# Performance work log

Hardware: AMD Instinct MI355X
Metric: run time of the kernel (lower is better)

## Reference

```python
import jax, jax.numpy as jnp
import numpy as np

B, N, E = 64, 256, 8192


def setup_inputs() -> dict:
    key = jax.random.key(0)
    k1, k2, k3, k4, k5 = jax.random.split(key, 5)
    P = jax.random.uniform(k1, (B, N, N), dtype=jnp.float32)
    d_error = jax.random.uniform(k2, (N, N), dtype=jnp.float32)
    edge_i = jax.random.randint(k3, (B, E), 0, N, dtype=jnp.int32)
    edge_j = jax.random.randint(k4, (B, E), 0, N, dtype=jnp.int32)
    edge_w = jax.random.uniform(k5, (B, E), dtype=jnp.float32)
    return {"P": P, "d_error": d_error, "edge_i": edge_i,
            "edge_j": edge_j, "edge_w": edge_w}


def reference(P, d_error, edge_i, edge_j, edge_w):
    # cost_e = P[b, i_e, :] @ d_error @ P[b, j_e, :]
    # Precompute Q = P @ d_error once, then gather per edge (memory-bound).
    Q = jnp.einsum('bin,nm->bim', P, d_error)            # [B, N, N]
    Qi = jnp.take_along_axis(Q, edge_i[:, :, None], axis=1)   # [B, E, N]
    Pj = jnp.take_along_axis(P, edge_j[:, :, None], axis=1)   # [B, E, N]
    cost = jnp.sum(Qi * Pj, axis=-1)                      # [B, E]
    sample_loss = jnp.sum(edge_w * cost, axis=-1)         # [B]
    sample_weight = jnp.maximum(jnp.sum(edge_w, axis=-1), 1e-8)
    # every sample has edges -> valid_samples == B, i.e. a mean over batch
    return jnp.mean(sample_loss / sample_weight)
```

## Files before the change

kernel.cpp:

```cpp
#include <hip/hip_runtime.h>

#define NN 256
#define BB 64
#define EE 8192

typedef __attribute__((ext_vector_type(8))) short bf16x8;
typedef __attribute__((ext_vector_type(8))) unsigned short u16x8;
typedef __attribute__((ext_vector_type(4))) float f32x4;

__device__ __forceinline__ unsigned short f2bf(float f) {
  union { float f; unsigned u; } x; x.f = f;
  unsigned r = x.u + 0x7FFFu + ((x.u >> 16) & 1u);
  return (unsigned short)(r >> 16);
}

__device__ __forceinline__ float bf2f(unsigned short h) {
  union { unsigned u; float f; } x; x.u = ((unsigned)h) << 16;
  return x.f;
}

__global__ __launch_bounds__(256) void transposeD(const float* __restrict__ D,
                                                  unsigned short* __restrict__ Dt) {
  __shared__ float t[32][33];
  int bx = blockIdx.x & 7;
  int by = blockIdx.x >> 3;
  int c = threadIdx.x & 31, r0 = threadIdx.x >> 5;
#pragma unroll
  for (int p = 0; p < 4; ++p) {
    int row = r0 + p * 8;
    t[row][c] = D[(bx * 32 + row) * NN + by * 32 + c];
  }
  __syncthreads();
#pragma unroll
  for (int p = 0; p < 4; ++p) {
    int row = r0 + p * 8;
    Dt[(by * 32 + row) * NN + bx * 32 + c] = f2bf(t[c][row]);
  }
}

__global__ __launch_bounds__(256) void gemm1(const float* __restrict__ P,
                                             const unsigned short* __restrict__ Dt,
                                             unsigned short* __restrict__ Qbf) {
  __shared__ __align__(16) unsigned short As[4096];
  __shared__ __align__(16) unsigned short Bs[4096];
  const int tid = threadIdx.x;
  const int b = blockIdx.x >> 2;
  const int tile = blockIdx.x & 3;
  const int ty = tile >> 1, tx = tile & 1;
  const int rowBase = ty * 128, colBase = tx * 128;

  const float4* Ag4 = (const float4*)(P + b * NN * NN);

  f32x4 acc[4][4];
#pragma unroll
  for (int i = 0; i < 4; ++i)
#pragma unroll
    for (int j = 0; j < 4; ++j) acc[i][j] = (f32x4){0.f, 0.f, 0.f, 0.f};

  const int lane = tid & 63;
  const int wave = tid >> 6;
  const int wr = (wave >> 1) * 64, wc = (wave & 1) * 64;
  const int frm = lane & 15;
  const int fq = (lane >> 4) * 8;

  const int arow0 = tid >> 3, af4 = tid & 7;
  const int brow0 = tid >> 2, bch = tid & 3;

  float4 ra[4];
  u16x8 rb[2];
#pragma unroll
  for (int i = 0; i < 4; ++i)
    ra[i] = Ag4[(rowBase + arow0 + i * 32) * 64 + 0 * 8 + af4];
#pragma unroll
  for (int i = 0; i < 2; ++i)
    rb[i] = *(const u16x8*)(Dt + (colBase + brow0 + i * 64) * NN + 0 * 32 + bch * 8);

  for (int ks = 0; ks < 8; ++ks) {
    __syncthreads();
#pragma unroll
    for (int i = 0; i < 4; ++i) {
      ushort4 o;
      o.x = f2bf(ra[i].x); o.y = f2bf(ra[i].y); o.z = f2bf(ra[i].z); o.w = f2bf(ra[i].w);
      *(ushort4*)(As + (arow0 + i * 32) * 32 + af4 * 4) = o;
    }
#pragma unroll
    for (int i = 0; i < 2; ++i)
      *(u16x8*)(Bs + (brow0 + i * 64) * 32 + bch * 8) = rb[i];
    __syncthreads();
    if (ks < 7) {
      const int k0 = (ks + 1) * 32;
#pragma unroll
      for (int i = 0; i < 4; ++i)
        ra[i] = Ag4[(rowBase + arow0 + i * 32) * 64 + (k0 >> 2) + af4];
#pragma unroll
      for (int i = 0; i < 2; ++i)
        rb[i] = *(const u16x8*)(Dt + (colBase + brow0 + i * 64) * NN + k0 + bch * 8);
    }
    bf16x8 af[4], bfr[4];
#pragma unroll
    for (int t = 0; t < 4; ++t) {
      af[t]  = *(const bf16x8*)(As + (wr + t * 16 + frm) * 32 + fq);
      bfr[t] = *(const bf16x8*)(Bs + (wc + t * 16 + frm) * 32 + fq);
    }
#pragma unroll
    for (int tr = 0; tr < 4; ++tr)
#pragma unroll
      for (int tc = 0; tc < 4; ++tc)
        acc[tr][tc] = __builtin_amdgcn_mfma_f32_16x16x32_bf16(af[tr], bfr[tc],
                                                              acc[tr][tc], 0, 0, 0);
  }

  unsigned short* outB = Qbf + b * NN * NN;
#pragma unroll
  for (int tr = 0; tr < 4; ++tr)
#pragma unroll
    for (int tc = 0; tc < 4; ++tc)
#pragma unroll
      for (int r = 0; r < 4; ++r) {
        int rg = rowBase + wr + tr * 16 + (lane >> 4) * 4 + r;
        int cg = colBase + wc + tc * 16 + (lane & 15);
        outB[rg * NN + cg] = f2bf(acc[tr][tc][r]);
      }
}

__global__ __launch_bounds__(256) void gemm2_fused(const unsigned short* __restrict__ Qbf,
                                                   const float* __restrict__ P,
                                                   const int* __restrict__ ei,
                                                   const int* __restrict__ ej,
                                                   const float* __restrict__ ew,
                                                   float* __restrict__ out) {
  __shared__ __align__(16) unsigned short As[4096];
  __shared__ __align__(16) unsigned short Bs[4096];
  __shared__ __align__(16) unsigned short Mt[128 * 130];
  __shared__ float red[8];
  const int tid = threadIdx.x;
  const int b = blockIdx.x >> 2;
  const int tile = blockIdx.x & 3;
  const int ty = tile >> 1, tx = tile & 1;
  const int rowBase = ty * 128, colBase = tx * 128;

  const unsigned short* Ag = Qbf + b * NN * NN;
  const float4* Bg4 = (const float4*)(P + b * NN * NN);

  f32x4 acc[4][4];
#pragma unroll
  for (int i = 0; i < 4; ++i)
#pragma unroll
    for (int j = 0; j < 4; ++j) acc[i][j] = (f32x4){0.f, 0.f, 0.f, 0.f};

  const int lane = tid & 63;
  const int wave = tid >> 6;
  const int wr = (wave >> 1) * 64, wc = (wave & 1) * 64;
  const int frm = lane & 15;
  const int fq = (lane >> 4) * 8;

  const int arow0 = tid >> 2, ach = tid & 3;
  const int brow0 = tid >> 3, bf4 = tid & 7;

  u16x8 ra[2];
  float4 rb[4];
#pragma unroll
  for (int i = 0; i < 2; ++i)
    ra[i] = *(const u16x8*)(Ag + (rowBase + arow0 + i * 64) * NN + ach * 8);
#pragma unroll
  for (int i = 0; i < 4; ++i)
    rb[i] = Bg4[(colBase + brow0 + i * 32) * 64 + bf4];

  for (int ks = 0; ks < 8; ++ks) {
    __syncthreads();
#pragma unroll
    for (int i = 0; i < 2; ++i)
      *(u16x8*)(As + (arow0 + i * 64) * 32 + ach * 8) = ra[i];
#pragma unroll
    for (int i = 0; i < 4; ++i) {
      ushort4 o;
      o.x = f2bf(rb[i].x); o.y = f2bf(rb[i].y); o.z = f2bf(rb[i].z); o.w = f2bf(rb[i].w);
      *(ushort4*)(Bs + (brow0 + i * 32) * 32 + bf4 * 4) = o;
    }
    __syncthreads();
    if (ks < 7) {
      const int k0 = (ks + 1) * 32;
#pragma unroll
      for (int i = 0; i < 2; ++i)
        ra[i] = *(const u16x8*)(Ag + (rowBase + arow0 + i * 64) * NN + k0 + ach * 8);
#pragma unroll
      for (int i = 0; i < 4; ++i)
        rb[i] = Bg4[(colBase + brow0 + i * 32) * 64 + (k0 >> 2) + bf4];
    }
    bf16x8 af[4], bfr[4];
#pragma unroll
    for (int t = 0; t < 4; ++t) {
      af[t]  = *(const bf16x8*)(As + (wr + t * 16 + frm) * 32 + fq);
      bfr[t] = *(const bf16x8*)(Bs + (wc + t * 16 + frm) * 32 + fq);
    }
#pragma unroll
    for (int tr = 0; tr < 4; ++tr)
#pragma unroll
      for (int tc = 0; tc < 4; ++tc)
        acc[tr][tc] = __builtin_amdgcn_mfma_f32_16x16x32_bf16(af[tr], bfr[tc],
                                                              acc[tr][tc], 0, 0, 0);
  }

#pragma unroll
  for (int tr = 0; tr < 4; ++tr)
#pragma unroll
    for (int tc = 0; tc < 4; ++tc)
#pragma unroll
      for (int r = 0; r < 4; ++r) {
        int rl = wr + tr * 16 + (lane >> 4) * 4 + r;
        int cl = wc + tc * 16 + (lane & 15);
        Mt[rl * 130 + cl] = f2bf(acc[tr][tc][r]);
      }
  __syncthreads();

  float lsum = 0.f, wsum = 0.f;
  const int2*   ei2 = (const int2*)(ei + b * EE);
  const int2*   ej2 = (const int2*)(ej + b * EE);
  const float2* ew2 = (const float2*)(ew + b * EE);
#pragma unroll 4
  for (int s = 0; s < 16; ++s) {
    int idx = s * 256 + tid;
    int2 ii = ei2[idx];
    int2 jj = ej2[idx];
    float2 ww = ew2[idx];
    wsum += ww.x + ww.y;
    int il = ii.x - rowBase, jl = jj.x - colBase;
    if (((unsigned)il < 128u) && ((unsigned)jl < 128u))
      lsum += ww.x * bf2f(Mt[il * 130 + jl]);
    il = ii.y - rowBase; jl = jj.y - colBase;
    if (((unsigned)il < 128u) && ((unsigned)jl < 128u))
      lsum += ww.y * bf2f(Mt[il * 130 + jl]);
  }
#pragma unroll
  for (int o = 32; o; o >>= 1) {
    lsum += __shfl_down(lsum, o);
    wsum += __shfl_down(wsum, o);
  }
  if (lane == 0) { red[wave] = lsum; red[4 + wave] = wsum; }
  __syncthreads();
  if (tid == 0) {
    float l = red[0] + red[1] + red[2] + red[3];
    float w = red[4] + red[5] + red[6] + red[7];
    atomicAdd(out, l / (64.0f * fmaxf(w, 1e-8f)));
  }
}

extern "C" void kernel_launch(void* const* d_in, const int* in_sizes, int n_in,
                              void* d_out, int out_size, void* d_ws, size_t ws_size,
                              hipStream_t stream) {
  const float* P  = (const float*)d_in[0];
  const float* D  = (const float*)d_in[1];
  const int*   ei = (const int*)d_in[2];
  const int*   ej = (const int*)d_in[3];
  const float* ew = (const float*)d_in[4];
  float* out = (float*)d_out;

  char* ws = (char*)d_ws;
  unsigned short* Qbf = (unsigned short*)ws;
  unsigned short* Dt  = (unsigned short*)(ws + 8388608);

  hipMemsetAsync(out, 0, out_size * sizeof(float), stream);
  transposeD<<<64, 256, 0, stream>>>(D, Dt);
  gemm1<<<256, 256, 0, stream>>>(P, Dt, Qbf);
  gemm2_fused<<<256, 256, 0, stream>>>(Qbf, P, ei, ej, ew, out);
}
```

Baseline: 102.5 us.

## Fuse both GEMMs into one kernel keeping Q tile in shared memory

Merges gemm1 and gemm2_fused into a single kernel. Each block computes its 128x256 strip of Q = P·D in registers and stores it as bf16 in LDS, then multiplies by the P^T tile and gathers edges from LDS. This removes the Q round-trip through global memory and one launch. The memset is folded into the transpose kernel, and edge loads are widened to int4. In exchange, each block recomputes the Q rows shared with its sibling tile, doubling the first GEMM's work. The larger LDS footprint and accumulator set limit occupancy to one block per CU.

New measurement: 97.21 us. -5.2%, faster.

```diff
diff --git a/kernel.cpp b/kernel.cpp
--- a/kernel.cpp
+++ b/kernel.cpp
@@ -3,6 +3,7 @@
 #define NN 256
 #define BB 64
 #define EE 8192
+#define TS_LD 264
 
 typedef __attribute__((ext_vector_type(8))) short bf16x8;
 typedef __attribute__((ext_vector_type(8))) unsigned short u16x8;
@@ -20,7 +21,9 @@
 }
 
 __global__ __launch_bounds__(256) void transposeD(const float* __restrict__ D,
-                                                  unsigned short* __restrict__ Dt) {
+                                                  unsigned short* __restrict__ Dt,
+                                                  float* __restrict__ out) {
+  if (blockIdx.x == 0 && threadIdx.x == 0) out[0] = 0.0f;
   __shared__ float t[32][33];
   int bx = blockIdx.x & 7;
   int by = blockIdx.x >> 3;
@@ -38,44 +41,54 @@
   }
 }
 
-__global__ __launch_bounds__(256) void gemm1(const float* __restrict__ P,
-                                             const unsigned short* __restrict__ Dt,
-                                             unsigned short* __restrict__ Qbf) {
-  __shared__ __align__(16) unsigned short As[4096];
-  __shared__ __align__(16) unsigned short Bs[4096];
+__global__ __launch_bounds__(256, 1) void fused(const float* __restrict__ P,
+                                                const unsigned short* __restrict__ Dt,
+                                                const int* __restrict__ ei,
+                                                const int* __restrict__ ej,
+                                                const float* __restrict__ ew,
+                                                float* __restrict__ out) {
+  __shared__ __align__(16) unsigned short As[128 * 32];
+  __shared__ __align__(16) unsigned short Bs[256 * 32];
+  __shared__ __align__(16) unsigned short Ts[128 * TS_LD];
+  __shared__ float red[8];
+
   const int tid = threadIdx.x;
   const int b = blockIdx.x >> 2;
   const int tile = blockIdx.x & 3;
   const int ty = tile >> 1, tx = tile & 1;
   const int rowBase = ty * 128, colBase = tx * 128;
 
-  const float4* Ag4 = (const float4*)(P + b * NN * NN);
-
-  f32x4 acc[4][4];
-#pragma unroll
-  for (int i = 0; i < 4; ++i)
-#pragma unroll
-    for (int j = 0; j < 4; ++j) acc[i][j] = (f32x4){0.f, 0.f, 0.f, 0.f};
-
   const int lane = tid & 63;
   const int wave = tid >> 6;
   const int wr = (wave >> 1) * 64, wc = (wave & 1) * 64;
   const int frm = lane & 15;
   const int fq = (lane >> 4) * 8;
+  const int crow = (lane >> 4) * 4;
+  const int ccol = lane & 15;
+
+  const float4* Pb4 = (const float4*)(P + b * NN * NN);
 
   const int arow0 = tid >> 3, af4 = tid & 7;
   const int brow0 = tid >> 2, bch = tid & 3;
 
+  f32x4 acc[4][8];
+#pragma unroll
+  for (int i = 0; i < 4; ++i)
+#pragma unroll
+    for (int j = 0; j < 8; ++j) acc[i][j] = (f32x4){0.f, 0.f, 0.f, 0.f};
+
   float4 ra[4];
-  u16x8 rb[2];
-#pragma unroll
-  for (int i = 0; i < 4; ++i)
-    ra[i] = Ag4[(rowBase + arow0 + i * 32) * 64 + 0 * 8 + af4];
-#pragma unroll
-  for (int i = 0; i < 2; ++i)
-    rb[i] = *(const u16x8*)(Dt + (colBase + brow0 + i * 64) * NN + 0 * 32 + bch * 8);
-
-  for (int ks = 0; ks < 8; ++ks) {
+  u16x8 rb[4];
+  float4 pb[4];
+#pragma unroll
+  for (int i = 0; i < 4; ++i)
+    ra[i] = Pb4[(rowBase + arow0 + i * 32) * 64 + af4];
+#pragma unroll
+  for (int i = 0; i < 4; ++i)
+    rb[i] = *(const u16x8*)(Dt + (brow0 + i * 64) * NN + bch * 8);
+
+  for (int s = 0; s < 8; ++s) {
+    const int k0 = s * 32;
     __syncthreads();
 #pragma unroll
     for (int i = 0; i < 4; ++i) {
@@ -84,22 +97,76 @@
       *(ushort4*)(As + (arow0 + i * 32) * 32 + af4 * 4) = o;
     }
 #pragma unroll
-    for (int i = 0; i < 2; ++i)
+    for (int i = 0; i < 4; ++i)
       *(u16x8*)(Bs + (brow0 + i * 64) * 32 + bch * 8) = rb[i];
     __syncthreads();
-    if (ks < 7) {
-      const int k0 = (ks + 1) * 32;
-#pragma unroll
-      for (int i = 0; i < 4; ++i)
-        ra[i] = Ag4[(rowBase + arow0 + i * 32) * 64 + (k0 >> 2) + af4];
-#pragma unroll
-      for (int i = 0; i < 2; ++i)
-        rb[i] = *(const u16x8*)(Dt + (colBase + brow0 + i * 64) * NN + k0 + bch * 8);
+    if (s < 7) {
+      const int k1 = k0 + 32;
+#pragma unroll
+      for (int i = 0; i < 4; ++i)
+        ra[i] = Pb4[(rowBase + arow0 + i * 32) * 64 + (k1 >> 2) + af4];
+#pragma unroll
+      for (int i = 0; i < 4; ++i)
+        rb[i] = *(const u16x8*)(Dt + (brow0 + i * 64) * NN + k1 + bch * 8);
+    } else {
+#pragma unroll
+      for (int i = 0; i < 4; ++i)
+        pb[i] = Pb4[(colBase + arow0 + i * 32) * 64 + af4];
+    }
+    bf16x8 af[4], bfr[8];
+#pragma unroll
+    for (int t = 0; t < 4; ++t)
+      af[t] = *(const bf16x8*)(As + (wr + t * 16 + frm) * 32 + fq);
+#pragma unroll
+    for (int h = 0; h < 2; ++h)
+#pragma unroll
+      for (int t = 0; t < 4; ++t)
+        bfr[h * 4 + t] = *(const bf16x8*)(Bs + (h * 128 + wc + t * 16 + frm) * 32 + fq);
+#pragma unroll
+    for (int tr = 0; tr < 4; ++tr)
+#pragma unroll
+      for (int j = 0; j < 8; ++j)
+        acc[tr][j] = __builtin_amdgcn_mfma_f32_16x16x32_bf16(af[tr], bfr[j],
+                                                             acc[tr][j], 0, 0, 0);
+  }
+
+#pragma unroll
+  for (int tr = 0; tr < 4; ++tr)
+#pragma unroll
+    for (int h = 0; h < 2; ++h)
+#pragma unroll
+      for (int tc = 0; tc < 4; ++tc)
+#pragma unroll
+        for (int r = 0; r < 4; ++r) {
+          int rl = wr + tr * 16 + crow + r;
+          int cl = h * 128 + wc + tc * 16 + ccol;
+          Ts[rl * TS_LD + cl] = f2bf(acc[tr][h * 4 + tc][r]);
+        }
+
+#pragma unroll
+  for (int i = 0; i < 4; ++i)
+#pragma unroll
+    for (int j = 0; j < 4; ++j) acc[i][j] = (f32x4){0.f, 0.f, 0.f, 0.f};
+
+  for (int s = 0; s < 8; ++s) {
+    const int k0 = s * 32;
+    __syncthreads();
+#pragma unroll
+    for (int i = 0; i < 4; ++i) {
+      ushort4 o;
+      o.x = f2bf(pb[i].x); o.y = f2bf(pb[i].y); o.z = f2bf(pb[i].z); o.w = f2bf(pb[i].w);
+      *(ushort4*)(Bs + (arow0 + i * 32) * 32 + af4 * 4) = o;
+    }
+    __syncthreads();
+    if (s < 7) {
+#pragma unroll
+      for (int i = 0; i < 4; ++i)
+        pb[i] = Pb4[(colBase + arow0 + i * 32) * 64 + ((k0 + 32) >> 2) + af4];
     }
     bf16x8 af[4], bfr[4];
 #pragma unroll
     for (int t = 0; t < 4; ++t) {
-      af[t]  = *(const bf16x8*)(As + (wr + t * 16 + frm) * 32 + fq);
+      af[t]  = *(const bf16x8*)(Ts + (wr + t * 16 + frm) * TS_LD + k0 + fq);
       bfr[t] = *(const bf16x8*)(Bs + (wc + t * 16 + frm) * 32 + fq);
     }
 #pragma unroll
@@ -110,126 +177,38 @@
                                                               acc[tr][tc], 0, 0, 0);
   }
 
-  unsigned short* outB = Qbf + b * NN * NN;
 #pragma unroll
   for (int tr = 0; tr < 4; ++tr)
 #pragma unroll
     for (int tc = 0; tc < 4; ++tc)
 #pragma unroll
       for (int r = 0; r < 4; ++r) {
-        int rg = rowBase + wr + tr * 16 + (lane >> 4) * 4 + r;
-        int cg = colBase + wc + tc * 16 + (lane & 15);
-        outB[rg * NN + cg] = f2bf(acc[tr][tc][r]);
-      }
-}
-
-__global__ __launch_bounds__(256) void gemm2_fused(const unsigned short* __restrict__ Qbf,
-                                                   const float* __restrict__ P,
-                                                   const int* __restrict__ ei,
-                                                   const int* __restrict__ ej,
-                                                   const float* __restrict__ ew,
-                                                   float* __restrict__ out) {
-  __shared__ __align__(16) unsigned short As[4096];
-  __shared__ __align__(16) unsigned short Bs[4096];
-  __shared__ __align__(16) unsigned short Mt[128 * 130];
-  __shared__ float red[8];
-  const int tid = threadIdx.x;
-  const int b = blockIdx.x >> 2;
-  const int tile = blockIdx.x & 3;
-  const int ty = tile >> 1, tx = tile & 1;
-  const int rowBase = ty * 128, colBase = tx * 128;
-
-  const unsigned short* Ag = Qbf + b * NN * NN;
-  const float4* Bg4 = (const float4*)(P + b * NN * NN);
-
-  f32x4 acc[4][4];
-#pragma unroll
-  for (int i = 0; i < 4; ++i)
-#pragma unroll
-    for (int j = 0; j < 4; ++j) acc[i][j] = (f32x4){0.f, 0.f, 0.f, 0.f};
-
-  const int lane = tid & 63;
-  const int wave = tid >> 6;
-  const int wr = (wave >> 1) * 64, wc = (wave & 1) * 64;
-  const int frm = lane & 15;
-  const int fq = (lane >> 4) * 8;
-
-  const int arow0 = tid >> 2, ach = tid & 3;
-  const int brow0 = tid >> 3, bf4 = tid & 7;
-
-  u16x8 ra[2];
-  float4 rb[4];
-#pragma unroll
-  for (int i = 0; i < 2; ++i)
-    ra[i] = *(const u16x8*)(Ag + (rowBase + arow0 + i * 64) * NN + ach * 8);
-#pragma unroll
-  for (int i = 0; i < 4; ++i)
-    rb[i] = Bg4[(colBase + brow0 + i * 32) * 64 + bf4];
-
-  for (int ks = 0; ks < 8; ++ks) {
-    __syncthreads();
-#pragma unroll
-    for (int i = 0; i < 2; ++i)
-      *(u16x8*)(As + (arow0 + i * 64) * 32 + ach * 8) = ra[i];
-#pragma unroll
-    for (int i = 0; i < 4; ++i) {
-      ushort4 o;
-      o.x = f2bf(rb[i].x); o.y = f2bf(rb[i].y); o.z = f2bf(rb[i].z); o.w = f2bf(rb[i].w);
-      *(ushort4*)(Bs + (brow0 + i * 32) * 32 + bf4 * 4) = o;
-    }
-    __syncthreads();
-    if (ks < 7) {
-      const int k0 = (ks + 1) * 32;
-#pragma unroll
-      for (int i = 0; i < 2; ++i)
-        ra[i] = *(const u16x8*)(Ag + (rowBase + arow0 + i * 64) * NN + k0 + ach * 8);
-#pragma unroll
-      for (int i = 0; i < 4; ++i)
-        rb[i] = Bg4[(colBase + brow0 + i * 32) * 64 + (k0 >> 2) + bf4];
-    }
-    bf16x8 af[4], bfr[4];
-#pragma unroll
-    for (int t = 0; t < 4; ++t) {
-      af[t]  = *(const bf16x8*)(As + (wr + t * 16 + frm) * 32 + fq);
-      bfr[t] = *(const bf16x8*)(Bs + (wc + t * 16 + frm) * 32 + fq);
-    }
-#pragma unroll
-    for (int tr = 0; tr < 4; ++tr)
-#pragma unroll
-      for (int tc = 0; tc < 4; ++tc)
-        acc[tr][tc] = __builtin_amdgcn_mfma_f32_16x16x32_bf16(af[tr], bfr[tc],
-                                                              acc[tr][tc], 0, 0, 0);
-  }
-
-#pragma unroll
-  for (int tr = 0; tr < 4; ++tr)
-#pragma unroll
-    for (int tc = 0; tc < 4; ++tc)
-#pragma unroll
-      for (int r = 0; r < 4; ++r) {
-        int rl = wr + tr * 16 + (lane >> 4) * 4 + r;
-        int cl = wc + tc * 16 + (lane & 15);
-        Mt[rl * 130 + cl] = f2bf(acc[tr][tc][r]);
+        int rl = wr + tr * 16 + crow + r;
+        int cl = wc + tc * 16 + ccol;
+        Ts[rl * TS_LD + cl] = f2bf(acc[tr][tc][r]);
       }
   __syncthreads();
 
   float lsum = 0.f, wsum = 0.f;
-  const int2*   ei2 = (const int2*)(ei + b * EE);
-  const int2*   ej2 = (const int2*)(ej + b * EE);
-  const float2* ew2 = (const float2*)(ew + b * EE);
-#pragma unroll 4
-  for (int s = 0; s < 16; ++s) {
+  const int4*   ei4 = (const int4*)(ei + b * EE);
+  const int4*   ej4 = (const int4*)(ej + b * EE);
+  const float4* ew4 = (const float4*)(ew + b * EE);
+#pragma unroll 2
+  for (int s = 0; s < 8; ++s) {
     int idx = s * 256 + tid;
-    int2 ii = ei2[idx];
-    int2 jj = ej2[idx];
-    float2 ww = ew2[idx];
-    wsum += ww.x + ww.y;
-    int il = ii.x - rowBase, jl = jj.x - colBase;
-    if (((unsigned)il < 128u) && ((unsigned)jl < 128u))
-      lsum += ww.x * bf2f(Mt[il * 130 + jl]);
+    int4 ii = ei4[idx];
+    int4 jj = ej4[idx];
+    float4 ww = ew4[idx];
+    wsum += ww.x + ww.y + ww.z + ww.w;
+    int il, jl;
+    il = ii.x - rowBase; jl = jj.x - colBase;
+    if (((unsigned)il < 128u) && ((unsigned)jl < 128u)) lsum += ww.x * bf2f(Ts[il * TS_LD + jl]);
     il = ii.y - rowBase; jl = jj.y - colBase;
-    if (((unsigned)il < 128u) && ((unsigned)jl < 128u))
-      lsum += ww.y * bf2f(Mt[il * 130 + jl]);
+    if (((unsigned)il < 128u) && ((unsigned)jl < 128u)) lsum += ww.y * bf2f(Ts[il * TS_LD + jl]);
+    il = ii.z - rowBase; jl = jj.z - colBase;
+    if (((unsigned)il < 128u) && ((unsigned)jl < 128u)) lsum += ww.z * bf2f(Ts[il * TS_LD + jl]);
+    il = ii.w - rowBase; jl = jj.w - colBase;
+    if (((unsigned)il < 128u) && ((unsigned)jl < 128u)) lsum += ww.w * bf2f(Ts[il * TS_LD + jl]);
   }
 #pragma unroll
   for (int o = 32; o; o >>= 1) {
@@ -255,12 +234,8 @@
   const float* ew = (const float*)d_in[4];
   float* out = (float*)d_out;
 
-  char* ws = (char*)d_ws;
-  unsigned short* Qbf = (unsigned short*)ws;
-  unsigned short* Dt  = (unsigned short*)(ws + 8388608);
-
-  hipMemsetAsync(out, 0, out_size * sizeof(float), stream);
-  transposeD<<<64, 256, 0, stream>>>(D, Dt);
-  gemm1<<<256, 256, 0, stream>>>(P, Dt, Qbf);
-  gemm2_fused<<<256, 256, 0, stream>>>(Qbf, P, ei, ej, ew, out);
-}
+  unsigned short* Dt = (unsigned short*)d_ws;
+
+  transposeD<<<64, 256, 0, stream>>>(D, Dt, out);
+  fused<<<256, 256, 0, stream>>>(P, Dt, ei, ej, ew, out);
+}
```
